# Performance work log

Hardware: AMD Instinct MI355X
Metric: run time of the kernel (lower is better)

Reference implementation:

```python
import jax, jax.numpy as jnp
import numpy as np
from jax import lax

B, N_FEAT, TIME_LEN, SCALE = 16, 16, 64, 32
HID, FS, NH = 128, 4, 2
DH = HID // NH
H2 = TIME_LEN - 2 * (FS - 1)   # 58 after two VALID convs
W2 = SCALE - 2 * (FS - 1)      # 26
L = H2 * W2                    # 1508 sequence tokens
FACTOR = 5
U = min(FACTOR * int(np.ceil(np.log(L))), L)  # 40 = sample_k = n_top (ProbSparse)


def setup_inputs() -> dict:
    key = jax.random.key(0)
    ks = jax.random.split(key, 10)
    s = 0.05
    f32 = jnp.float32
    return {
        "x": jax.random.normal(ks[0], (B, N_FEAT, TIME_LEN, SCALE), f32),
        "conv1_w": jax.random.normal(ks[1], (HID, N_FEAT, FS, FS), f32) * s,
        "conv1_b": jnp.zeros((HID,), f32),
        "conv2_w": jax.random.normal(ks[2], (HID, HID, FS, FS), f32) * s,
        "conv2_b": jnp.zeros((HID,), f32),
        "wq": jax.random.normal(ks[3], (HID, HID), f32) * s,
        "bq": jnp.zeros((HID,), f32),
        "wk": jax.random.normal(ks[4], (HID, HID), f32) * s,
        "bk": jnp.zeros((HID,), f32),
        "wv": jax.random.normal(ks[5], (HID, HID), f32) * s,
        "bv": jnp.zeros((HID,), f32),
        "wo": jax.random.normal(ks[6], (HID, HID), f32) * s,
        "bo": jnp.zeros((HID,), f32),
        "index_sample": jax.random.randint(ks[7], (L, U), 0, L),
    }


def _conv(x, w, b):
    y = lax.conv_general_dilated(x, w, (1, 1), 'VALID',
                                 dimension_numbers=('NCHW', 'OIHW', 'NCHW'))
    return y + b[None, :, None, None]


def _prob_attn(Q, K, V, index_sample):
    # Q, K, V: [B, H, L, D]. ProbSparse: score only the top-U informative queries.
    K_sample = K[:, :, index_sample, :]                       # [B,H,L,U,D] (gather per query row)
    QK_sample = jnp.einsum('bhld,bhlud->bhlu', Q, K_sample)   # sampled scores
    M = QK_sample.max(-1) - QK_sample.sum(-1) / L             # sparsity measurement, [B,H,L]
    _, M_top = lax.top_k(M, U)                                # [B,H,U] selected query indices
    Q_red = jnp.take_along_axis(Q, M_top[..., None], axis=2)  # [B,H,U,D]
    scores = jnp.einsum('bhud,bhkd->bhuk', Q_red, K) / jnp.sqrt(jnp.float32(DH))
    attn = jax.nn.softmax(scores, axis=-1)                    # [B,H,U,L]
    upd = jnp.einsum('bhuk,bhkd->bhud', attn, V)              # [B,H,U,D]
    ctx = jnp.broadcast_to(V.mean(axis=2, keepdims=True), V.shape)  # initial context = mean(V)
    ba = jnp.arange(B)[:, None, None]
    ha = jnp.arange(NH)[None, :, None]
    return ctx.at[ba, ha, M_top].set(upd)                     # scatter updated rows


def reference(x, conv1_w, conv1_b, conv2_w, conv2_b, wq, bq, wk, bk, wv, bv, wo, bo, index_sample):
    h = jax.nn.relu(_conv(x, conv1_w, conv1_b))
    h = jax.nn.relu(_conv(h, conv2_w, conv2_b))        # [B, HID, H2, W2]
    seq = h.reshape(B, HID, L).transpose(0, 2, 1)      # [B, L, HID]

    def heads(w, b):
        return (seq @ w + b).reshape(B, L, NH, DH).transpose(0, 2, 1, 3)  # [B,H,L,D]

    Q, K, V = heads(wq, bq), heads(wk, bk), heads(wv, bv)
    ctx = _prob_attn(Q, K, V, index_sample)            # [B,H,L,D]
    out = ctx.transpose(0, 2, 1, 3).reshape(B, L, HID)
    return out @ wo + bo                               # [B, L, HID]
```

## Files before the change

### kernel.cpp

```cpp
#include <hip/hip_runtime.h>
#include <hip/hip_bf16.h>

#define B_     16
#define NFEAT  16
#define TLEN   64
#define SCL    32
#define HID_   128
#define FS_    4
#define NH_    2
#define DH_    64
#define H1_    61
#define W1_    29
#define H2_    58
#define W2_    26
#define L_     1508
#define L4_    377
#define U_     40
#define M1_    28304
#define M2_    24128
#define GL_    48256

typedef unsigned short u16;
typedef __attribute__((ext_vector_type(8))) short short8v;
typedef __attribute__((ext_vector_type(16))) float f32x16;

__device__ inline unsigned bf16rne_u(float f) {
    unsigned u = __float_as_uint(f);
    return (u + 0x7FFFu + ((u >> 16) & 1u)) >> 16;
}
__device__ inline void split2(float f, u16& h, u16& l) {
    unsigned r = bf16rne_u(f);
    h = (u16)r;
    float hf = __uint_as_float((r & 0xFFFFu) << 16);
    unsigned r2 = bf16rne_u(f - hf);
    l = (u16)r2;
}


__global__ __launch_bounds__(256) void xpose_x_split(const float* __restrict__ x,
                                                     u16* __restrict__ xh,
                                                     u16* __restrict__ xl) {
    int idx = blockIdx.x * 256 + threadIdx.x;
    if (idx >= B_ * NFEAT * TLEN * SCL) return;
    int xx = idx & 31; int t = idx >> 5;
    int y  = t & 63;   t >>= 6;
    int ic = t & 15;   int b = t >> 4;
    u16 h, l;
    split2(x[idx], h, l);
    size_t dst = (((size_t)(b * TLEN + y) * SCL + xx) * NFEAT) + ic;
    xh[dst] = h; xl[dst] = l;
}

template <int CIN>
__global__ __launch_bounds__(256) void prep_cw(const float* __restrict__ w,
                                               u16* __restrict__ wh,
                                               u16* __restrict__ wl) {
    const int K = CIN * 16;
    int idx = blockIdx.x * 256 + threadIdx.x;
    if (idx >= 128 * K) return;
    int co = idx / K, k = idx - co * K;
    int ic = k % CIN, s = k / CIN;
    int fy = s >> 2, fx = s & 3;
    u16 h, l;
    split2(w[((co * CIN + ic) * FS_ + fy) * FS_ + fx], h, l);
    wh[idx] = h; wl[idx] = l;
}

__global__ __launch_bounds__(256) void prep_mw(const float* __restrict__ w,
                                               u16* __restrict__ wh,
                                               u16* __restrict__ wl) {
    int idx = blockIdx.x * 256 + threadIdx.x;
    if (idx >= 128 * 128) return;
    int n = idx >> 7, k = idx & 127;
    u16 h, l;
    split2(w[k * 128 + n], h, l);
    wh[idx] = h; wl[idx] = l;
}

template <int ASRC, int ABF, int OSTORE, bool RELU,
          int CIN, int HIN, int WIN, int HOUT, int WOUT>
__global__ __launch_bounds__(256, 2) void mgemm_k(const void* __restrict__ Ahv,
                                                  const void* __restrict__ Alv,
                                                  const u16* __restrict__ Bhg,
                                                  const u16* __restrict__ Blg,
                                                  const float* __restrict__ bias,
                                                  void* __restrict__ C0v,
                                                  void* __restrict__ C1v,
                                                  int Mrows, int K) {
    __shared__ u16 Ah_s[128 * 64];
    __shared__ u16 Al_s[128 * 64];
    __shared__ u16 Bh_s[128 * 64];
    __shared__ u16 Bl_s[128 * 64];

    const int tid = threadIdx.x;
    const int m0 = blockIdx.x * 128;
    const int wv = tid >> 6, lane = tid & 63;
    const int wm = wv >> 1, wn = wv & 1;
    const int lr = lane & 31;
    const int kh = lane >> 5;

    f32x16 acc[2][2];
#pragma unroll
    for (int i = 0; i < 2; ++i)
#pragma unroll
        for (int j = 0; j < 2; ++j)
#pragma unroll
            for (int r = 0; r < 16; ++r) acc[i][j][r] = 0.f;

    for (int k0 = 0; k0 < K; k0 += 64) {
#pragma unroll
        for (int g = 0; g < 4; ++g) {
            int gi = tid + g * 256;
            int row = gi >> 3, c = gi & 7;
            int m = m0 + row;
            if (m >= Mrows) m = Mrows - 1;
            int k = k0 + c * 8;
            size_t src;
            if constexpr (ASRC == 0) {
                src = (size_t)m * K + k;
            } else {
                int bb = m / (HOUT * WOUT), r = m % (HOUT * WOUT);
                int y = r / WOUT, xx = r % WOUT;
                int slice = k / CIN, ic = k - slice * CIN;
                int fy = slice >> 2, fx = slice & 3;
                src = ((size_t)((bb * HIN + y + fy) * WIN) + (xx + fx)) * CIN + ic;
            }
            int dst = row * 64 + ((c ^ (row & 7)) * 8);
            if constexpr (ABF == 1) {
                *(short8v*)&Ah_s[dst] = *(const short8v*)((const u16*)Ahv + src);
                *(short8v*)&Al_s[dst] = *(const short8v*)((const u16*)Alv + src);
            } else {
                const float* Af = (const float*)Ahv;
                float vv[8];
                *(float4*)&vv[0] = *(const float4*)&Af[src];
                *(float4*)&vv[4] = *(const float4*)&Af[src + 4];
                short8v hv, lv;
#pragma unroll
                for (int j = 0; j < 8; ++j) {
                    u16 h, l;
                    split2(vv[j], h, l);
                    hv[j] = (short)h; lv[j] = (short)l;
                }
                *(short8v*)&Ah_s[dst] = hv;
                *(short8v*)&Al_s[dst] = lv;
            }
        }
#pragma unroll
        for (int i = 0; i < 4; ++i) {
            int s = tid + i * 256;
            int nn = s >> 3, c = s & 7;
            size_t src = (size_t)nn * K + k0 + c * 8;
            int dst = nn * 64 + ((c ^ (nn & 7)) * 8);
            *(short8v*)&Bh_s[dst] = *(const short8v*)&Bhg[src];
            *(short8v*)&Bl_s[dst] = *(const short8v*)&Blg[src];
        }
        __syncthreads();
#pragma unroll
        for (int ks = 0; ks < 4; ++ks) {
            const int ch = ks * 2 + kh;
            short8v ah[2], al[2], bh[2], bl[2];
#pragma unroll
            for (int mf = 0; mf < 2; ++mf) {
                int row = wm * 64 + mf * 32 + lr;
                int idx = row * 64 + ((ch ^ (row & 7)) * 8);
                ah[mf] = *(const short8v*)&Ah_s[idx];
                al[mf] = *(const short8v*)&Al_s[idx];
            }
#pragma unroll
            for (int nf = 0; nf < 2; ++nf) {
                int rn = wn * 64 + nf * 32 + lr;
                int idx = rn * 64 + ((ch ^ (rn & 7)) * 8);
                bh[nf] = *(const short8v*)&Bh_s[idx];
                bl[nf] = *(const short8v*)&Bl_s[idx];
            }
#pragma unroll
            for (int mf = 0; mf < 2; ++mf)
#pragma unroll
                for (int nf = 0; nf < 2; ++nf) {
                    acc[mf][nf] = __builtin_amdgcn_mfma_f32_32x32x16_bf16(
                        ah[mf], bh[nf], acc[mf][nf], 0, 0, 0);
                    acc[mf][nf] = __builtin_amdgcn_mfma_f32_32x32x16_bf16(
                        ah[mf], bl[nf], acc[mf][nf], 0, 0, 0);
                    acc[mf][nf] = __builtin_amdgcn_mfma_f32_32x32x16_bf16(
                        al[mf], bh[nf], acc[mf][nf], 0, 0, 0);
                }
        }
        __syncthreads();
    }

#pragma unroll
    for (int mf = 0; mf < 2; ++mf)
#pragma unroll
        for (int nf = 0; nf < 2; ++nf) {
            int n = wn * 64 + nf * 32 + lr;
            float bv = bias[n];
#pragma unroll
            for (int r = 0; r < 16; ++r) {
                int row = (r & 3) + 8 * (r >> 2) + 4 * kh;
                int m = m0 + wm * 64 + mf * 32 + row;
                if (m >= Mrows) continue;
                float t = acc[mf][nf][r] + bv;
                if (RELU) t = fmaxf(t, 0.f);
                if constexpr (OSTORE == 0) {
                    ((float*)C0v)[(size_t)m * 128 + n] = t;
                } else if constexpr (OSTORE == 1) {
                    int b = m / L_, l = m - b * L_;
                    int h = n >> 6, d = n & 63;
                    ((float*)C0v)[(((size_t)(b * NH_ + h) * L_ + l) << 6) + d] = t;
                } else {
                    u16 h, l;
                    split2(t, h, l);
                    ((u16*)C0v)[(size_t)m * 128 + n] = h;
                    ((u16*)C1v)[(size_t)m * 128 + n] = l;
                }
            }
        }
}

__global__ __launch_bounds__(256) void xposeK_k(const float* __restrict__ Kt,
                                                float* __restrict__ Kdt) {
    __shared__ float tile[32][33];
    int l0 = blockIdx.x * 32, d0 = blockIdx.y * 32, bh = blockIdx.z;
    int col = threadIdx.x & 31, rw = threadIdx.x >> 5;
#pragma unroll
    for (int r = 0; r < 4; ++r) {
        int l = l0 + rw + r * 8;
        if (l < L_) tile[rw + r * 8][col] = Kt[((size_t)bh * L_ + l) * 64 + d0 + col];
    }
    __syncthreads();
#pragma unroll
    for (int r = 0; r < 4; ++r) {
        int d = rw + r * 8;
        int l = l0 + col;
        if (l < L_) Kdt[((size_t)bh * 64 + d0 + d) * L_ + l] = tile[col][d];
    }
}

__global__ __launch_bounds__(256) void probscore3_k(const float* __restrict__ Q,
                                                    const float* __restrict__ Kt,
                                                    const int* __restrict__ idxs,
                                                    float* __restrict__ Mp) {
    int bh = blockIdx.x;
    int l  = blockIdx.y * 32 + (threadIdx.x >> 3);
    int uh = threadIdx.x & 7;
    if (l >= L_) return;
    int gl = bh * L_ + l;

    int idxr[5];
#pragma unroll
    for (int j = 0; j < 5; ++j) idxr[j] = idxs[l * U_ + uh * 5 + j];

    const float4* Q4  = (const float4*)Q + (size_t)gl * 16;
    const float4* Kb4 = (const float4*)Kt + (size_t)bh * L_ * 16;

    float acc[5];
#pragma unroll
    for (int j = 0; j < 5; ++j) acc[j] = 0.f;

#pragma unroll
    for (int dc = 0; dc < 4; ++dc) {
        float4 q0 = Q4[dc * 4 + 0];
        float4 q1 = Q4[dc * 4 + 1];
        float4 q2 = Q4[dc * 4 + 2];
        float4 q3 = Q4[dc * 4 + 3];
#pragma unroll
        for (int j = 0; j < 5; ++j) {
            const float4* kr = Kb4 + (size_t)idxr[j] * 16 + dc * 4;
            float4 a = kr[0], b = kr[1], c = kr[2], d = kr[3];
            float t = acc[j];
            t = fmaf(q0.x, a.x, t); t = fmaf(q0.y, a.y, t);
            t = fmaf(q0.z, a.z, t); t = fmaf(q0.w, a.w, t);
            t = fmaf(q1.x, b.x, t); t = fmaf(q1.y, b.y, t);
            t = fmaf(q1.z, b.z, t); t = fmaf(q1.w, b.w, t);
            t = fmaf(q2.x, c.x, t); t = fmaf(q2.y, c.y, t);
            t = fmaf(q2.z, c.z, t); t = fmaf(q2.w, c.w, t);
            t = fmaf(q3.x, d.x, t); t = fmaf(q3.y, d.y, t);
            t = fmaf(q3.z, d.z, t); t = fmaf(q3.w, d.w, t);
            acc[j] = t;
        }
    }
    float mx = -1e30f, sm = 0.f;
#pragma unroll
    for (int j = 0; j < 5; ++j) { mx = fmaxf(mx, acc[j]); sm += acc[j]; }
    Mp[(size_t)uh * GL_ + gl] = mx;
    Mp[(size_t)(8 + uh) * GL_ + gl] = sm;
}

__global__ __launch_bounds__(64) void topk_k(const float* __restrict__ Mp,
                                             int* __restrict__ Mtop) {
    __shared__ float sv[L_];
    int bh = blockIdx.x, lane = threadIdx.x;
    for (int i = lane; i < L_; i += 64) {
        int gl = bh * L_ + i;
        float mx = -1e30f, sm = 0.f;
#pragma unroll
        for (int uh = 0; uh < 8; ++uh) {
            mx = fmaxf(mx, Mp[(size_t)uh * GL_ + gl]);
            sm += Mp[(size_t)(8 + uh) * GL_ + gl];
        }
        sv[i] = mx - sm * (1.0f / (float)L_);
    }
    __syncthreads();
    for (int it = 0; it < U_; ++it) {
        float bv = -1e30f; int bi = 1 << 30;
        for (int i = lane; i < L_; i += 64) {
            float v = sv[i];
            if (v > bv || (v == bv && i < bi)) { bv = v; bi = i; }
        }
#pragma unroll
        for (int o = 32; o >= 1; o >>= 1) {
            float v2 = __shfl_xor(bv, o);
            int   i2 = __shfl_xor(bi, o);
            if (v2 > bv || (v2 == bv && i2 < bi)) { bv = v2; bi = i2; }
        }
        if (lane == 0) { Mtop[bh * U_ + it] = bi; sv[bi] = -1e30f; }
        __syncthreads();
    }
}

__global__ __launch_bounds__(256) void vmean_k(const float* __restrict__ V,
                                               float* __restrict__ Vm) {
    __shared__ float red[256];
    int bh = blockIdx.x;
    int d = threadIdx.x & 63, part = threadIdx.x >> 6;
    const float* Vb = V + (size_t)bh * L_ * 64;
    float s = 0.f;
    for (int l = part; l < L_; l += 4) s += Vb[l * 64 + d];
    red[threadIdx.x] = s;
    __syncthreads();
    if (part == 0) {
        s = red[d] + red[64 + d] + red[128 + d] + red[192 + d];
        Vm[bh * 64 + d] = s / (float)L_;
    }
}

__global__ __launch_bounds__(256) void fill_ctx_k(const float* __restrict__ Vm,
                                                  float* __restrict__ ctxp) {
    int idx = blockIdx.x * 256 + threadIdx.x;
    if (idx >= B_ * L_ * 32) return;
    int c4 = idx & 31;
    int bl = idx >> 5;
    int b = bl / L_;
    int h = c4 >> 4, d4 = (c4 & 15) * 4;
    float4 v = *(const float4*)&Vm[(b * 2 + h) * 64 + d4];
    *(float4*)&ctxp[(size_t)idx * 4] = v;
}

__global__ __launch_bounds__(256) void attn2_k(const float* __restrict__ Q,
                                               const float* __restrict__ Kdt,
                                               const float* __restrict__ V,
                                               const int* __restrict__ Mtop,
                                               float* __restrict__ ctxp) {
    __shared__ float4 s4buf[L4_];
    __shared__ float qs[64];
    __shared__ float red[256];
    __shared__ float bcast[2];
    float* s = (float*)s4buf;

    int tid = threadIdx.x;
    int bhu = blockIdx.x;
    int bh = bhu & 31, u = bhu >> 5;
    int b = bh >> 1, h = bh & 1;
    int qi = Mtop[bh * U_ + u];

    if (tid < 16) ((float4*)qs)[tid] = ((const float4*)Q)[((size_t)bh * L_ + qi) * 16 + tid];
    __syncthreads();

    const float4* K4 = (const float4*)Kdt + (size_t)bh * 64 * L4_;
    float mx = -1e30f;
    for (int s4i = tid; s4i < L4_; s4i += 256) {
        float4 acc = {0.f, 0.f, 0.f, 0.f};
#pragma unroll 8
        for (int d = 0; d < 64; ++d) {
            float4 k4 = K4[(size_t)d * L4_ + s4i];
            float qd = qs[d];
            acc.x = fmaf(qd, k4.x, acc.x);
            acc.y = fmaf(qd, k4.y, acc.y);
            acc.z = fmaf(qd, k4.z, acc.z);
            acc.w = fmaf(qd, k4.w, acc.w);
        }
        acc.x *= 0.125f; acc.y *= 0.125f; acc.z *= 0.125f; acc.w *= 0.125f;
        s4buf[s4i] = acc;
        mx = fmaxf(mx, fmaxf(fmaxf(acc.x, acc.y), fmaxf(acc.z, acc.w)));
    }
    red[tid] = mx;
    __syncthreads();
    if (tid < 64) {
        float m4 = fmaxf(fmaxf(red[tid], red[tid + 64]), fmaxf(red[tid + 128], red[tid + 192]));
#pragma unroll
        for (int o = 32; o >= 1; o >>= 1) m4 = fmaxf(m4, __shfl_xor(m4, o));
        if (tid == 0) bcast[0] = m4;
    }
    __syncthreads();
    float bmx = bcast[0];

    float ps = 0.f;
    for (int l = tid; l < L_; l += 256) {
        float e = __expf(s[l] - bmx);
        s[l] = e;
        ps += e;
    }
    red[tid] = ps;
    __syncthreads();
    if (tid < 64) {
        float s4s = red[tid] + red[tid + 64] + red[tid + 128] + red[tid + 192];
#pragma unroll
        for (int o = 32; o >= 1; o >>= 1) s4s += __shfl_xor(s4s, o);
        if (tid == 0) bcast[1] = s4s;
    }
    __syncthreads();
    float inv = 1.0f / bcast[1];

    int w = tid >> 6, lane = tid & 63;
    const float* Vb = V + (size_t)bh * L_ * 64;
    float acc = 0.f;
    for (int l = w; l < L_; l += 4) acc = fmaf(s[l], Vb[(size_t)l * 64 + lane], acc);
    red[tid] = acc;
    __syncthreads();
    if (w == 0) {
        float r = red[lane] + red[64 + lane] + red[128 + lane] + red[192 + lane];
        ctxp[((size_t)b * L_ + qi) * 128 + h * 64 + lane] = r * inv;
    }
}

extern "C" void kernel_launch(void* const* d_in, const int* in_sizes, int n_in,
                              void* d_out, int out_size, void* d_ws, size_t ws_size,
                              hipStream_t stream) {
    const float* x   = (const float*)d_in[0];
    const float* c1w = (const float*)d_in[1];
    const float* c1b = (const float*)d_in[2];
    const float* c2w = (const float*)d_in[3];
    const float* c2b = (const float*)d_in[4];
    const float* wq  = (const float*)d_in[5];
    const float* bq  = (const float*)d_in[6];
    const float* wk  = (const float*)d_in[7];
    const float* bk  = (const float*)d_in[8];
    const float* wv  = (const float*)d_in[9];
    const float* bv  = (const float*)d_in[10];
    const float* wo  = (const float*)d_in[11];
    const float* bo  = (const float*)d_in[12];
    const int* isamp = (const int*)d_in[13];
    float* out = (float*)d_out;

    char* cur = (char*)d_ws;
    auto alloc = [&](size_t bytes) {
        char* p = cur;
        cur += (bytes + 255) & ~(size_t)255;
        return p;
    };
    u16* xp_h  = (u16*)alloc(524288 * 2);
    u16* xp_l  = (u16*)alloc(524288 * 2);
    u16* wt1h  = (u16*)alloc(32768 * 2);
    u16* wt1l  = (u16*)alloc(32768 * 2);
    u16* wt2h  = (u16*)alloc(262144 * 2);
    u16* wt2l  = (u16*)alloc(262144 * 2);
    u16* wtqh  = (u16*)alloc(16384 * 2);
    u16* wtql  = (u16*)alloc(16384 * 2);
    u16* wtkh  = (u16*)alloc(16384 * 2);
    u16* wtkl  = (u16*)alloc(16384 * 2);
    u16* wtvh  = (u16*)alloc(16384 * 2);
    u16* wtvl  = (u16*)alloc(16384 * 2);
    u16* wtoh  = (u16*)alloc(16384 * 2);
    u16* wtol  = (u16*)alloc(16384 * 2);
    u16* h1_h  = (u16*)alloc(3622912 * 2);
    u16* h1_l  = (u16*)alloc(3622912 * 2);
    u16* seq_h = (u16*)alloc(3088384 * 2);
    u16* seq_l = (u16*)alloc(3088384 * 2);
    float* Q    = (float*)alloc(3088384 * 4);
    float* Kt   = (float*)alloc(3088384 * 4);
    float* V    = (float*)alloc(3088384 * 4);
    float* Vm   = (float*)alloc(2048 * 4);
    float* ctxp = (float*)alloc(3088384 * 4);
    int*   Mtop = (int*)alloc(1280 * 4);
    float* Kdt  = (float*)h1_h;
    float* Mp   = (float*)seq_h;

    xpose_x_split<<<2048, 256, 0, stream>>>(x, xp_h, xp_l);
    prep_cw<16><<<128, 256, 0, stream>>>(c1w, wt1h, wt1l);
    prep_cw<128><<<1024, 256, 0, stream>>>(c2w, wt2h, wt2l);
    prep_mw<<<64, 256, 0, stream>>>(wq, wtqh, wtql);
    prep_mw<<<64, 256, 0, stream>>>(wk, wtkh, wtkl);
    prep_mw<<<64, 256, 0, stream>>>(wv, wtvh, wtvl);
    prep_mw<<<64, 256, 0, stream>>>(wo, wtoh, wtol);

    mgemm_k<1, 1, 2, true, 16, 64, 32, 61, 29>
        <<<222, 256, 0, stream>>>(xp_h, xp_l, wt1h, wt1l, c1b, h1_h, h1_l, M1_, 256);
    mgemm_k<1, 1, 2, true, 128, 61, 29, 58, 26>
        <<<189, 256, 0, stream>>>(h1_h, h1_l, wt2h, wt2l, c2b, seq_h, seq_l, M2_, 2048);

    mgemm_k<0, 1, 1, false, 1, 1, 1, 1, 1>
        <<<189, 256, 0, stream>>>(seq_h, seq_l, wtqh, wtql, bq, Q, nullptr, M2_, 128);
    mgemm_k<0, 1, 1, false, 1, 1, 1, 1, 1>
        <<<189, 256, 0, stream>>>(seq_h, seq_l, wtkh, wtkl, bk, Kt, nullptr, M2_, 128);
    mgemm_k<0, 1, 1, false, 1, 1, 1, 1, 1>
        <<<189, 256, 0, stream>>>(seq_h, seq_l, wtvh, wtvl, bv, V, nullptr, M2_, 128);

    xposeK_k<<<dim3(48, 2, 32), 256, 0, stream>>>(Kt, Kdt);
    probscore3_k<<<dim3(32, 48), 256, 0, stream>>>(Q, Kt, isamp, Mp);
    topk_k<<<32, 64, 0, stream>>>(Mp, Mtop);
    vmean_k<<<32, 256, 0, stream>>>(V, Vm);
    fill_ctx_k<<<3016, 256, 0, stream>>>(Vm, ctxp);
    attn2_k<<<1280, 256, 0, stream>>>(Q, Kdt, V, Mtop, ctxp);

    mgemm_k<0, 0, 0, false, 1, 1, 1, 1, 1>
        <<<189, 256, 0, stream>>>(ctxp, nullptr, wtoh, wtol, bo, out, nullptr, M2_, 128);
}
```

Before: 612.5 us.

## Reduce sparsity score in-warp, sort-based top-k, batch 4 queries per attention block

The probscore kernel now finishes the max/sum reduction with warp shuffles and writes a single M value per row, so the 16-plane partial buffer is no longer needed. Top-k becomes a per-lane register odd-even sort over 64-bit keys (value plus inverted index), followed by 40 rounds of wave-wide argmax that pop from each lane's sorted list. This removes the 40 serial rescans of shared memory and the block barriers between them. The attention kernel handles four selected queries per block, so each K and V load is reused four times across 320 blocks instead of 1280. The cost is more registers and shared memory per block and fewer blocks to fill the GPU.

```diff
diff --git a/kernel.cpp b/kernel.cpp
--- a/kernel.cpp
+++ b/kernel.cpp
@@ -21,6 +21,7 @@
 #define GL_    48256
 
 typedef unsigned short u16;
+typedef unsigned long long u64;
 typedef __attribute__((ext_vector_type(8))) short short8v;
 typedef __attribute__((ext_vector_type(16))) float f32x16;
 
@@ -236,10 +237,10 @@
     }
 }
 
-__global__ __launch_bounds__(256) void probscore3_k(const float* __restrict__ Q,
+__global__ __launch_bounds__(256) void probscore4_k(const float* __restrict__ Q,
                                                     const float* __restrict__ Kt,
                                                     const int* __restrict__ idxs,
-                                                    float* __restrict__ Mp) {
+                                                    float* __restrict__ Mout) {
     int bh = blockIdx.x;
     int l  = blockIdx.y * 32 + (threadIdx.x >> 3);
     int uh = threadIdx.x & 7;
@@ -282,39 +283,61 @@
     float mx = -1e30f, sm = 0.f;
 #pragma unroll
     for (int j = 0; j < 5; ++j) { mx = fmaxf(mx, acc[j]); sm += acc[j]; }
-    Mp[(size_t)uh * GL_ + gl] = mx;
-    Mp[(size_t)(8 + uh) * GL_ + gl] = sm;
-}
-
-__global__ __launch_bounds__(64) void topk_k(const float* __restrict__ Mp,
-                                             int* __restrict__ Mtop) {
-    __shared__ float sv[L_];
+#pragma unroll
+    for (int o = 1; o < 8; o <<= 1) {
+        mx = fmaxf(mx, __shfl_xor(mx, o));
+        sm += __shfl_xor(sm, o);
+    }
+    if (uh == 0) Mout[gl] = mx - sm * (1.0f / (float)L_);
+}
+
+__global__ __launch_bounds__(64) void topk2_k(const float* __restrict__ M,
+                                              int* __restrict__ Mtop) {
+    __shared__ u64 sk[24][64];
     int bh = blockIdx.x, lane = threadIdx.x;
-    for (int i = lane; i < L_; i += 64) {
-        int gl = bh * L_ + i;
-        float mx = -1e30f, sm = 0.f;
-#pragma unroll
-        for (int uh = 0; uh < 8; ++uh) {
-            mx = fmaxf(mx, Mp[(size_t)uh * GL_ + gl]);
-            sm += Mp[(size_t)(8 + uh) * GL_ + gl];
-        }
-        sv[i] = mx - sm * (1.0f / (float)L_);
-    }
-    __syncthreads();
+
+    u64 k[24];
+#pragma unroll
+    for (int p = 0; p < 24; ++p) {
+        int el = p * 64 + lane;
+        u64 key = 0ULL;
+        if (el < L_) {
+            unsigned u = __float_as_uint(M[bh * L_ + el]);
+            u ^= (u & 0x80000000u) ? 0xFFFFFFFFu : 0x80000000u;
+            key = ((u64)u << 32) | (unsigned)(~el);
+        }
+        k[p] = key;
+    }
+#pragma unroll
+    for (int ph = 0; ph < 24; ++ph) {
+#pragma unroll
+        for (int j0 = 0; j0 < 12; ++j0) {
+            int j = j0 * 2 + (ph & 1);
+            if (j + 1 < 24) {
+                u64 a = k[j], b = k[j + 1];
+                k[j]     = a > b ? a : b;
+                k[j + 1] = a > b ? b : a;
+            }
+        }
+    }
+#pragma unroll
+    for (int p = 0; p < 24; ++p) sk[p][lane] = k[p];
+
+    u64 cur = k[0];
+    int ptr = 0;
     for (int it = 0; it < U_; ++it) {
-        float bv = -1e30f; int bi = 1 << 30;
-        for (int i = lane; i < L_; i += 64) {
-            float v = sv[i];
-            if (v > bv || (v == bv && i < bi)) { bv = v; bi = i; }
-        }
+        u64 best = cur; int bl = lane;
 #pragma unroll
         for (int o = 32; o >= 1; o >>= 1) {
-            float v2 = __shfl_xor(bv, o);
-            int   i2 = __shfl_xor(bi, o);
-            if (v2 > bv || (v2 == bv && i2 < bi)) { bv = v2; bi = i2; }
-        }
-        if (lane == 0) { Mtop[bh * U_ + it] = bi; sv[bi] = -1e30f; }
-        __syncthreads();
+            u64 ok = __shfl_xor(best, o);
+            int ol = __shfl_xor(bl, o);
+            if (ok > best) { best = ok; bl = ol; }
+        }
+        if (lane == 0) Mtop[bh * U_ + it] = (int)(~(unsigned)best);
+        if (lane == bl) {
+            ++ptr;
+            cur = (ptr < 24) ? sk[ptr][lane] : 0ULL;
+        }
     }
 }
 
@@ -346,80 +369,115 @@
     *(float4*)&ctxp[(size_t)idx * 4] = v;
 }
 
-__global__ __launch_bounds__(256) void attn2_k(const float* __restrict__ Q,
+__global__ __launch_bounds__(256) void attn4_k(const float* __restrict__ Q,
                                                const float* __restrict__ Kdt,
                                                const float* __restrict__ V,
                                                const int* __restrict__ Mtop,
                                                float* __restrict__ ctxp) {
-    __shared__ float4 s4buf[L4_];
-    __shared__ float qs[64];
-    __shared__ float red[256];
-    __shared__ float bcast[2];
-    float* s = (float*)s4buf;
+    __shared__ float4 s4buf[4][L4_];
+    __shared__ float qs[4][64];
+    __shared__ float red4[256 * 4];
+    __shared__ float bcast[8];
 
     int tid = threadIdx.x;
-    int bhu = blockIdx.x;
-    int bh = bhu & 31, u = bhu >> 5;
+    int bid = blockIdx.x;
+    int bh = bid & 31, ug = bid >> 5;
     int b = bh >> 1, h = bh & 1;
-    int qi = Mtop[bh * U_ + u];
-
-    if (tid < 16) ((float4*)qs)[tid] = ((const float4*)Q)[((size_t)bh * L_ + qi) * 16 + tid];
+
+    int qi[4];
+#pragma unroll
+    for (int j = 0; j < 4; ++j) qi[j] = Mtop[bh * U_ + ug * 4 + j];
+
+    if (tid < 64) {
+        int j = tid >> 4, q4 = tid & 15;
+        ((float4*)qs[j])[q4] = ((const float4*)Q)[((size_t)bh * L_ + qi[j]) * 16 + q4];
+    }
     __syncthreads();
 
     const float4* K4 = (const float4*)Kdt + (size_t)bh * 64 * L4_;
-    float mx = -1e30f;
+    float mx[4] = {-1e30f, -1e30f, -1e30f, -1e30f};
     for (int s4i = tid; s4i < L4_; s4i += 256) {
-        float4 acc = {0.f, 0.f, 0.f, 0.f};
+        float4 a0 = {0.f,0.f,0.f,0.f}, a1 = a0, a2 = a0, a3 = a0;
 #pragma unroll 8
         for (int d = 0; d < 64; ++d) {
             float4 k4 = K4[(size_t)d * L4_ + s4i];
-            float qd = qs[d];
-            acc.x = fmaf(qd, k4.x, acc.x);
-            acc.y = fmaf(qd, k4.y, acc.y);
-            acc.z = fmaf(qd, k4.z, acc.z);
-            acc.w = fmaf(qd, k4.w, acc.w);
-        }
-        acc.x *= 0.125f; acc.y *= 0.125f; acc.z *= 0.125f; acc.w *= 0.125f;
-        s4buf[s4i] = acc;
-        mx = fmaxf(mx, fmaxf(fmaxf(acc.x, acc.y), fmaxf(acc.z, acc.w)));
-    }
-    red[tid] = mx;
-    __syncthreads();
-    if (tid < 64) {
-        float m4 = fmaxf(fmaxf(red[tid], red[tid + 64]), fmaxf(red[tid + 128], red[tid + 192]));
+            float q0 = qs[0][d], q1 = qs[1][d], q2 = qs[2][d], q3 = qs[3][d];
+            a0.x = fmaf(q0, k4.x, a0.x); a0.y = fmaf(q0, k4.y, a0.y);
+            a0.z = fmaf(q0, k4.z, a0.z); a0.w = fmaf(q0, k4.w, a0.w);
+            a1.x = fmaf(q1, k4.x, a1.x); a1.y = fmaf(q1, k4.y, a1.y);
+            a1.z = fmaf(q1, k4.z, a1.z); a1.w = fmaf(q1, k4.w, a1.w);
+            a2.x = fmaf(q2, k4.x, a2.x); a2.y = fmaf(q2, k4.y, a2.y);
+            a2.z = fmaf(q2, k4.z, a2.z); a2.w = fmaf(q2, k4.w, a2.w);
+            a3.x = fmaf(q3, k4.x, a3.x); a3.y = fmaf(q3, k4.y, a3.y);
+            a3.z = fmaf(q3, k4.z, a3.z); a3.w = fmaf(q3, k4.w, a3.w);
+        }
+        float4 av[4] = {a0, a1, a2, a3};
+#pragma unroll
+        for (int j = 0; j < 4; ++j) {
+            float4 a = av[j];
+            a.x *= 0.125f; a.y *= 0.125f; a.z *= 0.125f; a.w *= 0.125f;
+            s4buf[j][s4i] = a;
+            mx[j] = fmaxf(mx[j], fmaxf(fmaxf(a.x, a.y), fmaxf(a.z, a.w)));
+        }
+    }
+#pragma unroll
+    for (int j = 0; j < 4; ++j) red4[tid * 4 + j] = mx[j];
+    __syncthreads();
+    {
+        int w = tid >> 6, lane = tid & 63;
+        float m4 = fmaxf(fmaxf(red4[lane * 4 + w], red4[(lane + 64) * 4 + w]),
+                         fmaxf(red4[(lane + 128) * 4 + w], red4[(lane + 192) * 4 + w]));
 #pragma unroll
         for (int o = 32; o >= 1; o >>= 1) m4 = fmaxf(m4, __shfl_xor(m4, o));
-        if (tid == 0) bcast[0] = m4;
-    }
-    __syncthreads();
-    float bmx = bcast[0];
-
-    float ps = 0.f;
+        if (lane == 0) bcast[w] = m4;
+    }
+    __syncthreads();
+    float bmx0 = bcast[0], bmx1 = bcast[1], bmx2 = bcast[2], bmx3 = bcast[3];
+
+    float ps[4] = {0.f, 0.f, 0.f, 0.f};
+    float* s0 = (float*)s4buf[0];
+    float* s1 = (float*)s4buf[1];
+    float* s2 = (float*)s4buf[2];
+    float* s3 = (float*)s4buf[3];
     for (int l = tid; l < L_; l += 256) {
-        float e = __expf(s[l] - bmx);
-        s[l] = e;
-        ps += e;
-    }
-    red[tid] = ps;
-    __syncthreads();
-    if (tid < 64) {
-        float s4s = red[tid] + red[tid + 64] + red[tid + 128] + red[tid + 192];
-#pragma unroll
-        for (int o = 32; o >= 1; o >>= 1) s4s += __shfl_xor(s4s, o);
-        if (tid == 0) bcast[1] = s4s;
-    }
-    __syncthreads();
-    float inv = 1.0f / bcast[1];
+        float e0 = __expf(s0[l] - bmx0); s0[l] = e0; ps[0] += e0;
+        float e1 = __expf(s1[l] - bmx1); s1[l] = e1; ps[1] += e1;
+        float e2 = __expf(s2[l] - bmx2); s2[l] = e2; ps[2] += e2;
+        float e3 = __expf(s3[l] - bmx3); s3[l] = e3; ps[3] += e3;
+    }
+#pragma unroll
+    for (int j = 0; j < 4; ++j) red4[tid * 4 + j] = ps[j];
+    __syncthreads();
+    {
+        int w = tid >> 6, lane = tid & 63;
+        float sm = red4[lane * 4 + w] + red4[(lane + 64) * 4 + w] +
+                   red4[(lane + 128) * 4 + w] + red4[(lane + 192) * 4 + w];
+#pragma unroll
+        for (int o = 32; o >= 1; o >>= 1) sm += __shfl_xor(sm, o);
+        if (lane == 0) bcast[4 + w] = 1.0f / sm;
+    }
+    __syncthreads();
 
     int w = tid >> 6, lane = tid & 63;
     const float* Vb = V + (size_t)bh * L_ * 64;
-    float acc = 0.f;
-    for (int l = w; l < L_; l += 4) acc = fmaf(s[l], Vb[(size_t)l * 64 + lane], acc);
-    red[tid] = acc;
+    float pacc[4] = {0.f, 0.f, 0.f, 0.f};
+    for (int l = w; l < L_; l += 4) {
+        float vv = Vb[(size_t)l * 64 + lane];
+        pacc[0] = fmaf(s0[l], vv, pacc[0]);
+        pacc[1] = fmaf(s1[l], vv, pacc[1]);
+        pacc[2] = fmaf(s2[l], vv, pacc[2]);
+        pacc[3] = fmaf(s3[l], vv, pacc[3]);
+    }
+#pragma unroll
+    for (int j = 0; j < 4; ++j) red4[tid * 4 + j] = pacc[j];
     __syncthreads();
     if (w == 0) {
-        float r = red[lane] + red[64 + lane] + red[128 + lane] + red[192 + lane];
-        ctxp[((size_t)b * L_ + qi) * 128 + h * 64 + lane] = r * inv;
+#pragma unroll
+        for (int j = 0; j < 4; ++j) {
+            float r = red4[lane * 4 + j] + red4[(lane + 64) * 4 + j] +
+                      red4[(lane + 128) * 4 + j] + red4[(lane + 192) * 4 + j];
+            ctxp[((size_t)b * L_ + qi[j]) * 128 + h * 64 + lane] = r * bcast[4 + j];
+        }
     }
 }
 
@@ -496,11 +554,11 @@
         <<<189, 256, 0, stream>>>(seq_h, seq_l, wtvh, wtvl, bv, V, nullptr, M2_, 128);
 
     xposeK_k<<<dim3(48, 2, 32), 256, 0, stream>>>(Kt, Kdt);
-    probscore3_k<<<dim3(32, 48), 256, 0, stream>>>(Q, Kt, isamp, Mp);
-    topk_k<<<32, 64, 0, stream>>>(Mp, Mtop);
+    probscore4_k<<<dim3(32, 48), 256, 0, stream>>>(Q, Kt, isamp, Mp);
+    topk2_k<<<32, 64, 0, stream>>>(Mp, Mtop);
     vmean_k<<<32, 256, 0, stream>>>(V, Vm);
     fill_ctx_k<<<3016, 256, 0, stream>>>(Vm, ctxp);
-    attn2_k<<<1280, 256, 0, stream>>>(Q, Kdt, V, Mtop, ctxp);
+    attn4_k<<<320, 256, 0, stream>>>(Q, Kdt, V, Mtop, ctxp);
 
     mgemm_k<0, 0, 0, false, 1, 1, 1, 1, 1>
         <<<189, 256, 0, stream>>>(ctxp, nullptr, wtoh, wtol, bo, out, nullptr, M2_, 128);
```

After: 517.5 us. 1.18x faster.
